# Kernel optimization log

Hardware: AMD Instinct MI355X
Metric: run time of the kernel (lower is better)

## Reference

```python
import jax, jax.numpy as jnp
import numpy as np

B, L, G, D = 32, 128, 64, 256
HD = 128; H = 2 * HD          # bidirectional LSTM hidden
N, K = 8, 4                   # nodes per graph, idx per node
NINP, NHID, NREL = 128, 32, 16
NTOK = 1000
E = B * N * N                 # all-pairs edges per graph, flattened
EPS = 1e-5


def setup_inputs() -> dict:
    key = jax.random.key(0)
    ks = jax.random.split(key, 40)
    rn = lambda i, shape, s: (s * jax.random.normal(ks[i], shape)).astype(jnp.float32)
    inp = {}
    inp["seq"] = jax.random.randint(ks[0], (B, L), 0, NTOK, dtype=jnp.int32)
    inp["pos2grp"] = jax.random.randint(ks[1], (B, L), 0, G, dtype=jnp.int32)
    inp["idx"] = jax.random.randint(ks[2], (B, N, K), 0, L, dtype=jnp.int32)
    ii = np.repeat(np.arange(N), N); jj = np.tile(np.arange(N), N)
    inp["u"] = jnp.asarray((np.arange(B)[:, None] * N + ii[None, :]).reshape(-1), dtype=jnp.int32)
    inp["v"] = jnp.asarray((np.arange(B)[:, None] * N + jj[None, :]).reshape(-1), dtype=jnp.int32)
    inp["mask"] = jax.random.uniform(ks[3], (E, NREL)) < 0.1
    inp["emb"] = rn(4, (NTOK, D), 1.0)
    # BiLSTM params (1 layer, 2 directions); gate order i,f,g,o
    inp["Wih_f"] = rn(5, (4 * HD, D), 0.05); inp["Whh_f"] = rn(6, (4 * HD, HD), 0.05)
    inp["bih_f"] = jnp.zeros((4 * HD,), jnp.float32); inp["bhh_f"] = jnp.zeros((4 * HD,), jnp.float32)
    inp["Wih_b"] = rn(7, (4 * HD, D), 0.05); inp["Whh_b"] = rn(8, (4 * HD, HD), 0.05)
    inp["bih_b"] = jnp.zeros((4 * HD,), jnp.float32); inp["bhh_b"] = jnp.zeros((4 * HD,), jnp.float32)
    inp["lin_src_w"] = rn(9, (NINP, H), 0.05); inp["lin_src_b"] = jnp.zeros((NINP,), jnp.float32)
    inp["lin_dst_w"] = rn(10, (NINP, H), 0.05); inp["lin_dst_b"] = jnp.zeros((NINP,), jnp.float32)
    inp["bn_src_g"] = jnp.ones((NINP,), jnp.float32); inp["bn_src_b"] = jnp.zeros((NINP,), jnp.float32)
    inp["bn_dst_g"] = jnp.ones((NINP,), jnp.float32); inp["bn_dst_b"] = jnp.zeros((NINP,), jnp.float32)
    inp["ntl_w"] = rn(11, (NREL, NHID, NINP, NINP), 0.001)
    inp["ntl_v"] = rn(12, (NREL, NHID, 2 * NINP), 0.001)
    inp["ntl_b"] = jnp.zeros((NREL, NHID, 1), jnp.float32)
    inp["ntl_u"] = rn(13, (NREL, 1, NHID), 0.001)
    inp["ntl_bn_g"] = jnp.ones((NREL * NHID,), jnp.float32)
    inp["ntl_bn_b"] = jnp.zeros((NREL * NHID,), jnp.float32)
    return inp


def _lstm(xs, Wih, Whh, bih, bhh):
    # xs: (T, B, D) -> (T, B, HD)
    nb = xs.shape[1]
    def step(carry, xt):
        h, c = carry
        g = xt @ Wih.T + h @ Whh.T + bih + bhh
        i, f, gg, o = jnp.split(g, 4, axis=-1)
        c = jax.nn.sigmoid(f) * c + jax.nn.sigmoid(i) * jnp.tanh(gg)
        h = jax.nn.sigmoid(o) * jnp.tanh(c)
        return (h, c), h
    init = (jnp.zeros((nb, HD), xs.dtype), jnp.zeros((nb, HD), xs.dtype))
    _, hs = jax.lax.scan(step, init, xs)
    return hs


def _bn(x, g, b):
    # training-mode BatchNorm1d over axis 0 (biased variance, as torch)
    m = x.mean(0)
    v = x.var(0)
    return (x - m) * jax.lax.rsqrt(v + EPS) * g + b


def _forward(emb, Wih_f, Whh_f, bih_f, bhh_f, Wih_b, Whh_b, bih_b, bhh_b,
             lin_src_w, lin_src_b, lin_dst_w, lin_dst_b,
             bn_src_g, bn_src_b, bn_dst_g, bn_dst_b,
             ntl_w, ntl_v, ntl_b, ntl_u, ntl_bn_g, ntl_bn_b,
             seq, pos2grp, idx, u, v):
    # 1) token embedding + scatter_sum into groups
    x_tok = emb[seq]                                         # (B,L,D)
    flat_ids = (pos2grp + jnp.arange(B, dtype=pos2grp.dtype)[:, None] * G).reshape(-1)
    x_grp = jax.ops.segment_sum(x_tok.reshape(B * L, D), flat_ids,
                                num_segments=B * G).reshape(B, G, D)
    # 2) BiLSTM over group sequence
    xs = x_grp.transpose(1, 0, 2)                            # (G,B,D)
    hf = _lstm(xs, Wih_f, Whh_f, bih_f, bhh_f)
    hb = _lstm(xs[::-1], Wih_b, Whh_b, bih_b, bhh_b)[::-1]
    h_grp = jnp.concatenate([hf, hb], -1).transpose(1, 0, 2) # (B,G,H)
    # 3) fancy-indexed gather h_grp[i, pos2grp[i, idx], :] + scatter_sum over K
    grp_of_idx = jnp.take_along_axis(pos2grp, idx.reshape(B, N * K), axis=1)
    h_sel = jnp.take_along_axis(h_grp, grp_of_idx[..., None], axis=1)  # (B,N*K,H)
    h = h_sel.reshape(B, N, K, H).sum(2).reshape(B * N, H)
    # 4) per-endpoint projection + batchnorm
    hd = _bn(h[u] @ lin_src_w.T + lin_src_b, bn_src_g, bn_src_b)  # (E,NINP)
    tl = _bn(h[v] @ lin_dst_w.T + lin_dst_b, bn_dst_g, bn_dst_b)
    # 5) neural tensor layer (bilinear=True)
    cat = jnp.concatenate([hd, tl], 1)                       # (E,2*NINP)
    linear = jnp.einsum('rhi,ei->rhe', ntl_v, cat)
    tmp = jnp.einsum('rhij,ei->rhej', ntl_w, hd)             # (NREL,NHID,E,NINP)
    bilinear = jnp.einsum('rhej,ej->rhe', tmp, tl)
    pre = bilinear + linear + ntl_b                          # (NREL,NHID,E)
    flat = pre.reshape(NREL * NHID, E).T                     # (E, NREL*NHID)
    act = jnp.tanh(_bn(flat, ntl_bn_g, ntl_bn_b).T.reshape(NREL, NHID, E))
    logit = jnp.einsum('rh,rhe->er', ntl_u[:, 0, :], act)    # (E,NREL)
    return logit


def reference(seq, pos2grp, idx, u, v, mask, emb,
              Wih_f, Whh_f, bih_f, bhh_f, Wih_b, Whh_b, bih_b, bhh_b,
              lin_src_w, lin_src_b, lin_dst_w, lin_dst_b,
              bn_src_g, bn_src_b, bn_dst_g, bn_dst_b,
              ntl_w, ntl_v, ntl_b, ntl_u, ntl_bn_g, ntl_bn_b):
    logit = _forward(emb, Wih_f, Whh_f, bih_f, bhh_f, Wih_b, Whh_b, bih_b, bhh_b,
                     lin_src_w, lin_src_b, lin_dst_w, lin_dst_b,
                     bn_src_g, bn_src_b, bn_dst_g, bn_dst_b,
                     ntl_w, ntl_v, ntl_b, ntl_u, ntl_bn_g, ntl_bn_b,
                     seq, pos2grp, idx, u, v)
    gt = logit > 0
    eq = gt == mask
    acc = eq.astype(jnp.float32).mean()
    gid = jnp.repeat(jnp.arange(B, dtype=jnp.int32), N * N)
    em = jax.ops.segment_min(jnp.all(eq, 1).astype(jnp.int32), gid, num_segments=B)
    emr = em.astype(jnp.float32).mean()
    nll_pos = -jnp.sum(jnp.where(mask, jax.nn.log_sigmoid(logit), 0.0)) / B
    nll_neg = -jnp.sum(jnp.where(mask, 0.0, jnp.log(1.0 + 1e-5 - jax.nn.sigmoid(logit)))) / B
    loss = nll_pos + nll_neg
    return logit, loss, acc, emr
```

## Files before the change

### kernel.cpp

```cpp
#include <hip/hip_runtime.h>
#include <math.h>

namespace {

constexpr int cB = 32, cL = 128, cG = 64, cD = 256;
constexpr int cHD = 128, cH = 256;
constexpr int cN = 8, cK = 4;
constexpr int cNI = 128, cRH = 512;
constexpr int cE = 2048;
constexpr float cEPS = 1e-5f;

typedef __bf16 bf16x8 __attribute__((ext_vector_type(8)));
typedef float f32x4 __attribute__((ext_vector_type(4)));

__device__ __forceinline__ f32x4 mfma16(bf16x8 a, bf16x8 b, f32x4 c) {
    return __builtin_amdgcn_mfma_f32_16x16x32_bf16(a, b, c, 0, 0, 0);
}

__device__ __forceinline__ float bf2f(unsigned short u) {
    unsigned int x = ((unsigned int)u) << 16;
    return __uint_as_float(x);
}
__device__ __forceinline__ unsigned short f2bf(float f) {
    unsigned int x = __float_as_uint(f);
    unsigned int r = (x + 0x7fffu + ((x >> 16) & 1u)) >> 16;
    return (unsigned short)r;
}
__device__ __forceinline__ float frcp(float x) { return __builtin_amdgcn_rcpf(x); }
__device__ __forceinline__ float fsig(float x) { return frcp(1.f + __expf(-x)); }
__device__ __forceinline__ float ftanh(float x) { return 1.f - 2.f * frcp(__expf(2.f * x) + 1.f); }
__device__ __forceinline__ float nls(float x) {
    return (x >= 0.f) ? log1pf(expf(-x)) : (log1pf(expf(x)) - x);
}

__device__ __forceinline__ void bar_lgkm() {
    asm volatile("s_waitcnt lgkmcnt(0)\n\ts_barrier" ::: "memory");
}

__global__ void k_embed(const int* __restrict__ seq, const int* __restrict__ p2g,
                        const float* __restrict__ emb, float* __restrict__ x_seq) {
    __shared__ float xl[cG * cD];
    int b = blockIdx.x, t = threadIdx.x;
    for (int g = 0; g < cG; ++g) xl[g * cD + t] = 0.f;
    for (int l = 0; l < cL; ++l) {
        int tok = seq[b * cL + l];
        int g = p2g[b * cL + l];
        xl[g * cD + t] += emb[tok * cD + t];
    }
    for (int g = 0; g < cG; ++g)
        x_seq[(g * cB + b) * cD + t] = xl[g * cD + t];
}

__global__ __launch_bounds__(256) void k_gemm_in(
    const float* __restrict__ x_seq,
    const float* __restrict__ wih_f, const float* __restrict__ wih_b,
    const float* __restrict__ bih_f, const float* __restrict__ bhh_f,
    const float* __restrict__ bih_b, const float* __restrict__ bhh_b,
    float* __restrict__ pre) {
    __shared__ float As[64][17];
    __shared__ float Bs[16][68];
    int t = threadIdx.x;
    int n0 = blockIdx.x * 64, m0 = blockIdx.y * 64;
    int tx = t & 15, ty = t >> 4;
    float acc[4][4] = {};
    for (int k0 = 0; k0 < cD; k0 += 16) {
        {
            int r = t >> 2, c = (t & 3) * 4;
            float4 a4 = *(const float4*)(x_seq + (size_t)(m0 + r) * cD + k0 + c);
            As[r][c + 0] = a4.x; As[r][c + 1] = a4.y; As[r][c + 2] = a4.z; As[r][c + 3] = a4.w;
        }
        {
            int n = t >> 2, c = (t & 3) * 4;
            int gn = n0 + n;
            const float* wrow = (gn < 512) ? (wih_f + (size_t)gn * cD)
                                           : (wih_b + (size_t)(gn - 512) * cD);
            float4 b4 = *(const float4*)(wrow + k0 + c);
            Bs[c + 0][n] = b4.x; Bs[c + 1][n] = b4.y; Bs[c + 2][n] = b4.z; Bs[c + 3][n] = b4.w;
        }
        __syncthreads();
#pragma unroll
        for (int k = 0; k < 16; ++k) {
            float a[4], bb[4];
#pragma unroll
            for (int i = 0; i < 4; ++i) a[i] = As[ty * 4 + i][k];
#pragma unroll
            for (int j = 0; j < 4; ++j) bb[j] = Bs[k][tx * 4 + j];
#pragma unroll
            for (int i = 0; i < 4; ++i)
#pragma unroll
                for (int j = 0; j < 4; ++j) acc[i][j] += a[i] * bb[j];
        }
        __syncthreads();
    }
#pragma unroll
    for (int i = 0; i < 4; ++i) {
        int m = m0 + ty * 4 + i;
        int g = m >> 5, b = m & 31;
        float4 v;
        float* vv = &v.x;
#pragma unroll
        for (int j = 0; j < 4; ++j) {
            int n = n0 + tx * 4 + j;
            float bias = (n < 512) ? (bih_f[n] + bhh_f[n]) : (bih_b[n - 512] + bhh_b[n - 512]);
            vv[j] = acc[i][j] + bias;
        }
        *(float4*)(pre + (((size_t)g * 256 + (n0 >> 2) + tx) * 32 + b) * 4) = v;
    }
}

__device__ __forceinline__ void lstm_step(
    f32x4 (&acc)[4], float (&cst)[4], const bf16x8 (&wf)[4][4],
    const unsigned short* __restrict__ hr, unsigned short* __restrict__ hw,
    const int (&rdo)[4], int wro,
    const float* __restrict__ preb, int gpre, bool dopre,
    unsigned short* __restrict__ hob, int g) {
    bf16x8 hf[4];
#pragma unroll
    for (int kf = 0; kf < 4; ++kf)
        hf[kf] = *(const bf16x8*)((const char*)hr + rdo[kf]);
#pragma unroll
    for (int kf = 0; kf < 4; ++kf)
#pragma unroll
        for (int q = 0; q < 4; ++q)
            acc[q] = mfma16(wf[q][kf], hf[kf], acc[q]);
    float hv[4];
#pragma unroll
    for (int r = 0; r < 4; ++r) {
        float ig = fsig(acc[0][r]);
        float fg = fsig(acc[1][r]);
        float gg = ftanh(acc[2][r]);
        float og = fsig(acc[3][r]);
        float cv = fg * cst[r] + ig * gg;
        cst[r] = cv;
        hv[r] = og * ftanh(cv);
    }
    if (dopre) {
#pragma unroll
        for (int q = 0; q < 4; ++q)
            acc[q] = *(const f32x4*)(preb + (size_t)gpre * 32768 + q * 4096);
    }
    unsigned int p0 = (unsigned int)f2bf(hv[0]) | ((unsigned int)f2bf(hv[1]) << 16);
    unsigned int p1 = (unsigned int)f2bf(hv[2]) | ((unsigned int)f2bf(hv[3]) << 16);
    *(uint2*)((char*)hw + wro) = make_uint2(p0, p1);
    *(uint2*)(hob + (size_t)g * 8192) = make_uint2(p0, p1);
    bar_lgkm();
}

__global__ __launch_bounds__(512, 2) void k_lstm_m(
    const float* __restrict__ pre,
    const float* __restrict__ whh_f, const float* __restrict__ whh_b,
    unsigned short* __restrict__ h_out) {
    __shared__ __align__(16) unsigned short hl[2][2048];
    int t = threadIdx.x;
    int w = t >> 6, l = t & 63, lc = l & 15, lk = l >> 4;
    int dir = blockIdx.x >> 1, bg = (blockIdx.x & 1) * 16;
    const float* whh = dir ? whh_b : whh_f;
    bf16x8 wf[4][4];
#pragma unroll
    for (int q = 0; q < 4; ++q) {
        int n = q * 128 + w * 16 + lc;
#pragma unroll
        for (int kf = 0; kf < 4; ++kf) {
            const float* src = whh + (size_t)n * 128 + kf * 32 + lk * 8;
            float4 s0 = *(const float4*)src, s1 = *(const float4*)(src + 4);
            bf16x8 v;
            v[0] = (__bf16)s0.x; v[1] = (__bf16)s0.y; v[2] = (__bf16)s0.z; v[3] = (__bf16)s0.w;
            v[4] = (__bf16)s1.x; v[5] = (__bf16)s1.y; v[6] = (__bf16)s1.z; v[7] = (__bf16)s1.w;
            wf[q][kf] = v;
        }
    }
    *(uint2*)&hl[1][t * 4] = make_uint2(0u, 0u);
    const float* preb = pre + ((size_t)(dir * 128 + w * 4 + lk) * 32 + (bg + lc)) * 4;
    unsigned short* hob = h_out + ((size_t)(dir * 32 + bg + lc) * 128 + w * 16 + lk * 4);
    int rdo[4];
#pragma unroll
    for (int kf = 0; kf < 4; ++kf)
        rdo[kf] = (lc * 256 + kf * 64 + lk * 16) ^ (lc << 4);
    int wro = (lc * 256 + w * 32 + lk * 8) ^ (lc << 4);
    f32x4 accA[4], accB[4];
    float cst[4] = {0.f, 0.f, 0.f, 0.f};
    int g0 = dir ? 63 : 0;
    int sgn = dir ? -1 : 1;
#pragma unroll
    for (int q = 0; q < 4; ++q) accA[q] = *(const f32x4*)(preb + (size_t)g0 * 32768 + q * 4096);
#pragma unroll
    for (int q = 0; q < 4; ++q) accB[q] = *(const f32x4*)(preb + (size_t)(g0 + sgn) * 32768 + q * 4096);
    bar_lgkm();
    for (int s = 0; s < 64; s += 2) {
        int ga = g0 + sgn * s;
        lstm_step(accA, cst, wf, hl[1], hl[0], rdo, wro, preb,
                  ga + 2 * sgn, s < 62, hob, ga);
        lstm_step(accB, cst, wf, hl[0], hl[1], rdo, wro, preb,
                  ga + 3 * sgn, s < 61, hob, ga + sgn);
    }
}

__global__ __launch_bounds__(256) void k_gather_proj(
    const int* __restrict__ idx, const int* __restrict__ p2g,
    const unsigned short* __restrict__ h_out,
    const float* __restrict__ w_src, const float* __restrict__ b_src,
    const float* __restrict__ w_dst, const float* __restrict__ b_dst,
    float* __restrict__ s_raw, float* __restrict__ d_raw) {
    int bn = blockIdx.x;
    int b = bn >> 3;
    int t = threadIdx.x;
    int dirq = t >> 7, hh = t & 127;
    __shared__ float xr[cH];
    float acc = 0.f;
#pragma unroll
    for (int k = 0; k < cK; ++k) {
        int l = idx[bn * cK + k];
        int g = p2g[b * cL + l];
        acc += bf2f(h_out[(size_t)g * 8192 + (size_t)(dirq * 32 + b) * 128 + hh]);
    }
    xr[t] = acc;
    __syncthreads();
    int which = t >> 7, c = t & 127;
    const float* w = which ? w_dst : w_src;
    const float* bb = which ? b_dst : b_src;
    const float* wr = w + (size_t)c * cH;
    float s = bb[c];
#pragma unroll 8
    for (int k = 0; k < cH; k += 4) {
        float4 w4 = *(const float4*)(wr + k);
        s += w4.x * xr[k] + w4.y * xr[k + 1] + w4.z * xr[k + 2] + w4.w * xr[k + 3];
    }
    (which ? d_raw : s_raw)[(size_t)bn * cNI + c] = s;
}

__global__ void k_bn_nodes(const float* __restrict__ s_raw, const float* __restrict__ d_raw,
                           const float* __restrict__ g_src, const float* __restrict__ b_src,
                           const float* __restrict__ g_dst, const float* __restrict__ b_dst,
                           float* __restrict__ hd_bn, float* __restrict__ tl_bn) {
    int ch = blockIdx.x, which = ch >> 7, cc = ch & 127;
    int t = threadIdx.x;
    const float* raw = which ? d_raw : s_raw;
    float v = raw[(size_t)t * cNI + cc];
    __shared__ float ssum[256], ssq[256];
    ssum[t] = v;
    ssq[t] = v * v;
    __syncthreads();
    for (int o = 128; o > 0; o >>= 1) {
        if (t < o) { ssum[t] += ssum[t + o]; ssq[t] += ssq[t + o]; }
        __syncthreads();
    }
    float mean = ssum[0] * (1.f / 256.f);
    float var = ssq[0] * (1.f / 256.f) - mean * mean;
    float gam = which ? g_dst[cc] : g_src[cc];
    float bet = which ? b_dst[cc] : b_src[cc];
    float scale = gam * rsqrtf(var + cEPS);
    (which ? tl_bn : hd_bn)[(size_t)t * cNI + cc] = (v - mean) * scale + bet;
}

__global__ __launch_bounds__(256, 2) void k_ntl_A(
    const float* __restrict__ hd_bn, const float* __restrict__ tl_bn,
    const float* __restrict__ ntl_w, const float* __restrict__ ntl_v,
    unsigned short* __restrict__ tmp,
    float* __restrict__ lsrc, float* __restrict__ ldst) {
    __shared__ __align__(16) unsigned short wl[128 * 128];
    __shared__ float vsh[256];
    int rh = blockIdx.x, t = threadIdx.x;
    int w = t >> 6, l = t & 63, lc = l & 15, lk = l >> 4;
    vsh[t] = ntl_v[(size_t)rh * 256 + t];
    {
        const float* wbase = ntl_w + (size_t)rh * 16384;
        int k = t >> 1, c0 = (t & 1) * 64;
        int sw = ((k >> 3) & 3) << 4;
#pragma unroll
        for (int u = 0; u < 8; ++u) {
            const float* src = wbase + k * 128 + c0 + u * 8;
            float4 f0 = *(const float4*)src, f1 = *(const float4*)(src + 4);
            bf16x8 v;
            v[0] = (__bf16)f0.x; v[1] = (__bf16)f0.y; v[2] = (__bf16)f0.z; v[3] = (__bf16)f0.w;
            v[4] = (__bf16)f1.x; v[5] = (__bf16)f1.y; v[6] = (__bf16)f1.z; v[7] = (__bf16)f1.w;
            *(bf16x8*)((char*)wl + ((k * 256 + (c0 + u * 8) * 2) ^ sw)) = v;
        }
    }
    __syncthreads();
    {
        const float* hr = hd_bn + (size_t)t * cNI;
        const float* tr = tl_bn + (size_t)t * cNI;
        float a1 = 0.f, a2 = 0.f;
#pragma unroll 8
        for (int i = 0; i < cNI; i += 4) {
            float4 h4 = *(const float4*)(hr + i);
            float4 t4 = *(const float4*)(tr + i);
            a1 += h4.x * vsh[i] + h4.y * vsh[i + 1] + h4.z * vsh[i + 2] + h4.w * vsh[i + 3];
            a2 += t4.x * vsh[128 + i] + t4.y * vsh[128 + i + 1] + t4.z * vsh[128 + i + 2] + t4.w * vsh[128 + i + 3];
        }
        lsrc[(size_t)rh * 256 + t] = a1;
        ldst[(size_t)rh * 256 + t] = a2;
    }
    f32x4 acc[4][8] = {};
#pragma unroll
    for (int kf = 0; kf < 4; ++kf) {
        bf16x8 af[4];
#pragma unroll
        for (int mt = 0; mt < 4; ++mt) {
            int m = w * 64 + mt * 16 + lc;
            const float* ap = hd_bn + (size_t)m * 128 + kf * 32 + lk * 8;
            float4 a0 = *(const float4*)ap, a1 = *(const float4*)(ap + 4);
            bf16x8 v;
            v[0] = (__bf16)a0.x; v[1] = (__bf16)a0.y; v[2] = (__bf16)a0.z; v[3] = (__bf16)a0.w;
            v[4] = (__bf16)a1.x; v[5] = (__bf16)a1.y; v[6] = (__bf16)a1.z; v[7] = (__bf16)a1.w;
            af[mt] = v;
        }
#pragma unroll
        for (int nt = 0; nt < 8; ++nt) {
            int kb = (kf * 32 + lk * 8) * 256;
            int jb = (nt * 16 + lc) * 2;
            bf16x8 bv = *(const bf16x8*)((char*)wl + ((kb + jb) ^ (lk << 4)));
#pragma unroll
            for (int mt = 0; mt < 4; ++mt) acc[mt][nt] = mfma16(af[mt], bv, acc[mt][nt]);
        }
    }
#pragma unroll
    for (int mt = 0; mt < 4; ++mt) {
#pragma unroll
        for (int nt = 0; nt < 8; ++nt) {
            unsigned int lo = (unsigned int)f2bf(acc[mt][nt][0]) | ((unsigned int)f2bf(acc[mt][nt][1]) << 16);
            unsigned int hi = (unsigned int)f2bf(acc[mt][nt][2]) | ((unsigned int)f2bf(acc[mt][nt][3]) << 16);
            size_t off = (size_t)rh * 32768 + (size_t)((((w * 4 + mt) * 8 + nt) * 64 + l) * 4);
            *(uint2*)(tmp + off) = make_uint2(lo, hi);
        }
    }
}

__global__ __launch_bounds__(256) void k_ntl_B(
    const unsigned short* __restrict__ tmp, const float* __restrict__ tl_bn,
    const float* __restrict__ lsrc, const float* __restrict__ ldst,
    const float* __restrict__ ntl_b, float* __restrict__ pre2) {
    int bgid = blockIdx.x;
    int rh = blockIdx.y;
    int t = threadIdx.x;
    int n0 = bgid * 32;
    __shared__ float tm[32][132];
    __shared__ float tl[32][132];
    {
        const uint4* src = (const uint4*)(tmp + (size_t)rh * 32768 +
                                          (size_t)(bgid >> 1) * 8192 + (size_t)(bgid & 1) * 4096);
#pragma unroll
        for (int rep = 0; rep < 2; ++rep) {
            int q = t + rep * 256;
            uint4 uv = src[q];
            unsigned int wds[4] = {uv.x, uv.y, uv.z, uv.w};
            int e0 = q * 8;
#pragma unroll
            for (int ui = 0; ui < 4; ++ui) {
                int e = e0 + ui * 2;
                int mt_l = e >> 11;
                int nt = (e >> 8) & 7;
                int ln = (e >> 2) & 63;
                int r = e & 3;
                int m = mt_l * 16 + (ln >> 4) * 4 + r;
                int j = nt * 16 + (ln & 15);
                tm[m][j] = bf2f((unsigned short)(wds[ui] & 0xffff));
                tm[m + 1][j] = bf2f((unsigned short)(wds[ui] >> 16));
            }
        }
        int r = t >> 3;
        int c0 = (t & 7) * 16;
        const float4* fsrc = (const float4*)(tl_bn + (size_t)(n0 + r) * cNI + c0);
        float4 f0 = fsrc[0], f1 = fsrc[1], f2v = fsrc[2], f3 = fsrc[3];
        float* frow = &tl[r][c0];
        frow[0] = f0.x; frow[1] = f0.y; frow[2] = f0.z; frow[3] = f0.w;
        frow[4] = f1.x; frow[5] = f1.y; frow[6] = f1.z; frow[7] = f1.w;
        frow[8] = f2v.x; frow[9] = f2v.y; frow[10] = f2v.z; frow[11] = f2v.w;
        frow[12] = f3.x; frow[13] = f3.y; frow[14] = f3.z; frow[15] = f3.w;
    }
    __syncthreads();
    int b_l = t >> 6, p = t & 63, i = p >> 3, j = p & 7;
    const float* ta = &tm[b_l * 8 + i][0];
    const float* tb = &tl[b_l * 8 + j][0];
    float s = 0.f;
#pragma unroll 8
    for (int k = 0; k < 128; ++k) s += ta[k] * tb[k];
    int e = bgid * 256 + t;
    int bglob = bgid * 4 + b_l;
    int un = bglob * 8 + i, vn = bglob * 8 + j;
    pre2[(size_t)rh * cE + e] = s + lsrc[(size_t)rh * 256 + un] + ldst[(size_t)rh * 256 + vn] + ntl_b[rh];
}

__global__ void k_bn2(const float* __restrict__ pre2,
                      const float* __restrict__ g, const float* __restrict__ bta,
                      float* __restrict__ scale, float* __restrict__ shift) {
    int rh = blockIdx.x, t = threadIdx.x;
    const float* row = pre2 + (size_t)rh * cE;
    float s = 0.f, q = 0.f;
#pragma unroll
    for (int ii = 0; ii < 8; ++ii) {
        float v = row[ii * 256 + t];
        s += v; q += v * v;
    }
    __shared__ float ssum[256], ssq[256];
    ssum[t] = s; ssq[t] = q;
    __syncthreads();
    for (int o = 128; o > 0; o >>= 1) {
        if (t < o) { ssum[t] += ssum[t + o]; ssq[t] += ssq[t + o]; }
        __syncthreads();
    }
    if (t == 0) {
        float mean = ssum[0] * (1.f / 2048.f);
        float var = ssq[0] * (1.f / 2048.f) - mean * mean;
        float sc = g[rh] * rsqrtf(var + cEPS);
        scale[rh] = sc;
        shift[rh] = bta[rh] - mean * sc;
    }
}

__global__ __launch_bounds__(256) void k_final(
    const float* __restrict__ pre2,
    const float* __restrict__ scale, const float* __restrict__ shift,
    const float* __restrict__ ntl_u, float* __restrict__ out) {
    int r = blockIdx.y;
    int e = blockIdx.x * 256 + threadIdx.x;
    float a = 0.f;
#pragma unroll
    for (int h = 0; h < 32; ++h) {
        int rh = r * 32 + h;
        float p = pre2[(size_t)rh * cE + e];
        a += ntl_u[rh] * ftanh(fmaf(p, scale[rh], shift[rh]));
    }
    out[(size_t)e * 16 + r] = a;
}

__global__ void k_loss(const float* __restrict__ out, const int* __restrict__ mask,
                       float* __restrict__ part) {
    int b = blockIdx.x, t = threadIdx.x;
    float nll = 0.f;
    int corr = 0, em = 1;
#pragma unroll
    for (int q = 0; q < 4; ++q) {
        int f = t * 4 + q;
        float x = out[(size_t)b * 1024 + f];
        int m = mask[(size_t)b * 1024 + f];
        bool gt = x > 0.f;
        bool mb = (m != 0);
        bool eq = (gt == mb);
        corr += eq ? 1 : 0;
        em &= eq ? 1 : 0;
        if (mb) nll += nls(x);
        else nll += -logf(1.f / (1.f + expf(x)) + 1e-5f);
    }
    __shared__ float rs[256];
    __shared__ int rc[256], re[256];
    rs[t] = nll; rc[t] = corr; re[t] = em;
    __syncthreads();
    for (int o = 128; o > 0; o >>= 1) {
        if (t < o) { rs[t] += rs[t + o]; rc[t] += rc[t + o]; re[t] &= re[t + o]; }
        __syncthreads();
    }
    if (t == 0) {
        part[b * 4 + 0] = rs[0];
        part[b * 4 + 1] = (float)rc[0];
        part[b * 4 + 2] = (float)re[0];
    }
}

__global__ void k_loss_fin(const float* __restrict__ part, float* __restrict__ out) {
    if (threadIdx.x == 0) {
        float nll = 0.f, corr = 0.f, em = 0.f;
        for (int b = 0; b < 32; ++b) {
            nll += part[b * 4 + 0];
            corr += part[b * 4 + 1];
            em += part[b * 4 + 2];
        }
        out[32768] = nll / 32.f;
        out[32769] = corr / 32768.f;
        out[32770] = em / 32.f;
    }
}

}

extern "C" void kernel_launch(void* const* d_in, const int* in_sizes, int n_in,
                              void* d_out, int out_size, void* d_ws, size_t ws_size,
                              hipStream_t stream) {
    (void)in_sizes; (void)n_in; (void)out_size; (void)ws_size;
    const int* seq = (const int*)d_in[0];
    const int* p2g = (const int*)d_in[1];
    const int* idx = (const int*)d_in[2];
    const int* mask = (const int*)d_in[5];
    const float* emb = (const float*)d_in[6];
    const float* wih_f = (const float*)d_in[7];
    const float* whh_f = (const float*)d_in[8];
    const float* bih_f = (const float*)d_in[9];
    const float* bhh_f = (const float*)d_in[10];
    const float* wih_b = (const float*)d_in[11];
    const float* whh_b = (const float*)d_in[12];
    const float* bih_b = (const float*)d_in[13];
    const float* bhh_b = (const float*)d_in[14];
    const float* lsw = (const float*)d_in[15];
    const float* lsb = (const float*)d_in[16];
    const float* ldw = (const float*)d_in[17];
    const float* ldb = (const float*)d_in[18];
    const float* bn_sg = (const float*)d_in[19];
    const float* bn_sb = (const float*)d_in[20];
    const float* bn_dg = (const float*)d_in[21];
    const float* bn_db = (const float*)d_in[22];
    const float* ntlw = (const float*)d_in[23];
    const float* ntlv = (const float*)d_in[24];
    const float* ntlb = (const float*)d_in[25];
    const float* ntlu = (const float*)d_in[26];
    const float* bn2g = (const float*)d_in[27];
    const float* bn2b = (const float*)d_in[28];
    float* out = (float*)d_out;
    char* ws = (char*)d_ws;

    float* x_seq = (float*)(ws + 0);
    float* pre = (float*)(ws + 2097152);
    unsigned short* tmp = (unsigned short*)(ws + 0);
    size_t off = 33554432;
    unsigned short* h_out = (unsigned short*)(ws + off); off += 1048576;
    float* s_raw = (float*)(ws + off); off += 131072;
    float* d_raw = (float*)(ws + off); off += 131072;
    float* hd_bn = (float*)(ws + off); off += 131072;
    float* tl_bn = (float*)(ws + off); off += 131072;
    float* lsrc = (float*)(ws + off); off += 524288;
    float* ldst = (float*)(ws + off); off += 524288;
    float* pre2 = (float*)(ws + off); off += 4194304;
    float* scale = (float*)(ws + off); off += 2048;
    float* shift = (float*)(ws + off); off += 2048;
    float* part = (float*)(ws + off); off += 512;

    k_embed<<<32, 256, 0, stream>>>(seq, p2g, emb, x_seq);
    k_gemm_in<<<dim3(16, 32), 256, 0, stream>>>(x_seq, wih_f, wih_b, bih_f, bhh_f, bih_b, bhh_b, pre);
    k_lstm_m<<<4, 512, 0, stream>>>(pre, whh_f, whh_b, h_out);
    k_gather_proj<<<256, 256, 0, stream>>>(idx, p2g, h_out, lsw, lsb, ldw, ldb, s_raw, d_raw);
    k_bn_nodes<<<256, 256, 0, stream>>>(s_raw, d_raw, bn_sg, bn_sb, bn_dg, bn_db, hd_bn, tl_bn);
    k_ntl_A<<<512, 256, 0, stream>>>(hd_bn, tl_bn, ntlw, ntlv, tmp, lsrc, ldst);
    k_ntl_B<<<dim3(8, 512), 256, 0, stream>>>(tmp, tl_bn, lsrc, ldst, ntlb, pre2);
    k_bn2<<<512, 256, 0, stream>>>(pre2, bn2g, bn2b, scale, shift);
    k_final<<<dim3(8, 16), 256, 0, stream>>>(pre2, scale, shift, ntlu, out);
    k_loss<<<32, 256, 0, stream>>>(out, mask, part);
    k_loss_fin<<<1, 32, 0, stream>>>(part, out);
}
```

Baseline: 183.2 us.

## Use MFMA for input GEMM, fuse projection with BN and loss into final kernel

The input-projection GEMM moves from a scalar FP32 LDS-tiled kernel to bf16 MFMA, with operands converted from global memory on the fly. The gather and projection are split into a transposed gather kernel and a per-channel projection kernel that also computes batch-norm statistics, which removes the separate BN kernel. The loss reduction is folded into k_final using wave ballots and shuffles, so the standalone loss kernel goes away. Together these cut kernel launches and scalar FP32 work, at the cost of bf16 rounding in the input GEMM and a gather stage that runs on only 8 blocks.

```diff
diff --git a/kernel.cpp b/kernel.cpp
--- a/kernel.cpp
+++ b/kernel.cpp
@@ -31,6 +31,13 @@
 __device__ __forceinline__ float ftanh(float x) { return 1.f - 2.f * frcp(__expf(2.f * x) + 1.f); }
 __device__ __forceinline__ float nls(float x) {
     return (x >= 0.f) ? log1pf(expf(-x)) : (log1pf(expf(x)) - x);
+}
+__device__ __forceinline__ bf16x8 cvt8(const float* __restrict__ p) {
+    float4 a = *(const float4*)p, b = *(const float4*)(p + 4);
+    bf16x8 v;
+    v[0] = (__bf16)a.x; v[1] = (__bf16)a.y; v[2] = (__bf16)a.z; v[3] = (__bf16)a.w;
+    v[4] = (__bf16)b.x; v[5] = (__bf16)b.y; v[6] = (__bf16)b.z; v[7] = (__bf16)b.w;
+    return v;
 }
 
 __device__ __forceinline__ void bar_lgkm() {
@@ -51,61 +58,46 @@
         x_seq[(g * cB + b) * cD + t] = xl[g * cD + t];
 }
 
-__global__ __launch_bounds__(256) void k_gemm_in(
+__global__ __launch_bounds__(512) void k_gemm_in(
     const float* __restrict__ x_seq,
     const float* __restrict__ wih_f, const float* __restrict__ wih_b,
     const float* __restrict__ bih_f, const float* __restrict__ bhh_f,
     const float* __restrict__ bih_b, const float* __restrict__ bhh_b,
     float* __restrict__ pre) {
-    __shared__ float As[64][17];
-    __shared__ float Bs[16][68];
+    int ns = blockIdx.x, g = blockIdx.y;
     int t = threadIdx.x;
-    int n0 = blockIdx.x * 64, m0 = blockIdx.y * 64;
-    int tx = t & 15, ty = t >> 4;
-    float acc[4][4] = {};
-    for (int k0 = 0; k0 < cD; k0 += 16) {
-        {
-            int r = t >> 2, c = (t & 3) * 4;
-            float4 a4 = *(const float4*)(x_seq + (size_t)(m0 + r) * cD + k0 + c);
-            As[r][c + 0] = a4.x; As[r][c + 1] = a4.y; As[r][c + 2] = a4.z; As[r][c + 3] = a4.w;
-        }
-        {
-            int n = t >> 2, c = (t & 3) * 4;
-            int gn = n0 + n;
-            const float* wrow = (gn < 512) ? (wih_f + (size_t)gn * cD)
-                                           : (wih_b + (size_t)(gn - 512) * cD);
-            float4 b4 = *(const float4*)(wrow + k0 + c);
-            Bs[c + 0][n] = b4.x; Bs[c + 1][n] = b4.y; Bs[c + 2][n] = b4.z; Bs[c + 3][n] = b4.w;
-        }
-        __syncthreads();
-#pragma unroll
-        for (int k = 0; k < 16; ++k) {
-            float a[4], bb[4];
-#pragma unroll
-            for (int i = 0; i < 4; ++i) a[i] = As[ty * 4 + i][k];
-#pragma unroll
-            for (int j = 0; j < 4; ++j) bb[j] = Bs[k][tx * 4 + j];
-#pragma unroll
-            for (int i = 0; i < 4; ++i)
-#pragma unroll
-                for (int j = 0; j < 4; ++j) acc[i][j] += a[i] * bb[j];
-        }
-        __syncthreads();
-    }
-#pragma unroll
-    for (int i = 0; i < 4; ++i) {
-        int m = m0 + ty * 4 + i;
-        int g = m >> 5, b = m & 31;
-        float4 v;
-        float* vv = &v.x;
-#pragma unroll
-        for (int j = 0; j < 4; ++j) {
-            int n = n0 + tx * 4 + j;
-            float bias = (n < 512) ? (bih_f[n] + bhh_f[n]) : (bih_b[n - 512] + bhh_b[n - 512]);
-            vv[j] = acc[i][j] + bias;
-        }
-        *(float4*)(pre + (((size_t)g * 256 + (n0 >> 2) + tx) * 32 + b) * 4) = v;
-    }
+    int w = t >> 6, l = t & 63, lc = l & 15, lk = l >> 4;
+    int gn = ns * 128 + w * 16 + lc;
+    const float* wrow = (gn < 512) ? (wih_f + (size_t)gn * cD)
+                                   : (wih_b + (size_t)(gn - 512) * cD);
+    const float* xb0 = x_seq + ((size_t)g * 32 + lc) * cD;
+    const float* xb1 = x_seq + ((size_t)g * 32 + 16 + lc) * cD;
+    f32x4 acc0 = {0.f, 0.f, 0.f, 0.f}, acc1 = {0.f, 0.f, 0.f, 0.f};
+#pragma unroll
+    for (int kf = 0; kf < 8; ++kf) {
+        int ko = kf * 32 + lk * 8;
+        bf16x8 a = cvt8(wrow + ko);
+        bf16x8 b0 = cvt8(xb0 + ko);
+        bf16x8 b1 = cvt8(xb1 + ko);
+        acc0 = mfma16(a, b0, acc0);
+        acc1 = mfma16(a, b1, acc1);
+    }
+    int nb = ns * 128 + w * 16 + lk * 4;
+    float4 bv;
+    if (nb < 512) {
+        float4 u = *(const float4*)(bih_f + nb);
+        float4 v = *(const float4*)(bhh_f + nb);
+        bv = make_float4(u.x + v.x, u.y + v.y, u.z + v.z, u.w + v.w);
+    } else {
+        float4 u = *(const float4*)(bih_b + nb - 512);
+        float4 v = *(const float4*)(bhh_b + nb - 512);
+        bv = make_float4(u.x + v.x, u.y + v.y, u.z + v.z, u.w + v.w);
+    }
+    size_t base = ((size_t)g * 256 + (nb >> 2)) * 32;
+    *(float4*)(pre + (base + lc) * 4) =
+        make_float4(acc0[0] + bv.x, acc0[1] + bv.y, acc0[2] + bv.z, acc0[3] + bv.w);
+    *(float4*)(pre + (base + 16 + lc) * 4) =
+        make_float4(acc1[0] + bv.x, acc1[1] + bv.y, acc1[2] + bv.z, acc1[3] + bv.w);
 }
 
 __device__ __forceinline__ void lstm_step(
@@ -160,14 +152,8 @@
     for (int q = 0; q < 4; ++q) {
         int n = q * 128 + w * 16 + lc;
 #pragma unroll
-        for (int kf = 0; kf < 4; ++kf) {
-            const float* src = whh + (size_t)n * 128 + kf * 32 + lk * 8;
-            float4 s0 = *(const float4*)src, s1 = *(const float4*)(src + 4);
-            bf16x8 v;
-            v[0] = (__bf16)s0.x; v[1] = (__bf16)s0.y; v[2] = (__bf16)s0.z; v[3] = (__bf16)s0.w;
-            v[4] = (__bf16)s1.x; v[5] = (__bf16)s1.y; v[6] = (__bf16)s1.z; v[7] = (__bf16)s1.w;
-            wf[q][kf] = v;
-        }
+        for (int kf = 0; kf < 4; ++kf)
+            wf[q][kf] = cvt8(whh + (size_t)n * 128 + kf * 32 + lk * 8);
     }
     *(uint2*)&hl[1][t * 4] = make_uint2(0u, 0u);
     const float* preb = pre + ((size_t)(dir * 128 + w * 4 + lk) * 32 + (bg + lc)) * 4;
@@ -188,57 +174,55 @@
     bar_lgkm();
     for (int s = 0; s < 64; s += 2) {
         int ga = g0 + sgn * s;
-        lstm_step(accA, cst, wf, hl[1], hl[0], rdo, wro, preb,
-                  ga + 2 * sgn, s < 62, hob, ga);
-        lstm_step(accB, cst, wf, hl[0], hl[1], rdo, wro, preb,
-                  ga + 3 * sgn, s < 61, hob, ga + sgn);
-    }
-}
-
-__global__ __launch_bounds__(256) void k_gather_proj(
+        lstm_step(accA, cst, wf, hl[1], hl[0], rdo, wro, preb, ga + 2 * sgn, s < 62, hob, ga);
+        lstm_step(accB, cst, wf, hl[0], hl[1], rdo, wro, preb, ga + 3 * sgn, s < 61, hob, ga + sgn);
+    }
+}
+
+__global__ __launch_bounds__(256) void k_gather(
     const int* __restrict__ idx, const int* __restrict__ p2g,
-    const unsigned short* __restrict__ h_out,
+    const unsigned short* __restrict__ h_out, float* __restrict__ hsumT) {
+    __shared__ float xr[32][257];
+    int n0 = blockIdx.x * 32, t = threadIdx.x;
+    int dirq = t >> 7, hh = t & 127;
+    for (int nl = 0; nl < 32; ++nl) {
+        int bn = n0 + nl;
+        int b = bn >> 3;
+        float acc = 0.f;
+#pragma unroll
+        for (int k = 0; k < cK; ++k) {
+            int l = idx[bn * cK + k];
+            int g = p2g[b * cL + l];
+            acc += bf2f(h_out[(size_t)g * 8192 + (size_t)(dirq * 32 + b) * 128 + hh]);
+        }
+        xr[nl][t] = acc;
+    }
+    __syncthreads();
+    int c_hi = t >> 5, nl = t & 31;
+    for (int rep = 0; rep < 32; ++rep) {
+        int c = rep * 8 + c_hi;
+        hsumT[(size_t)c * 256 + n0 + nl] = xr[nl][c];
+    }
+}
+
+__global__ __launch_bounds__(256) void k_proj_bn(
+    const float* __restrict__ hsumT,
     const float* __restrict__ w_src, const float* __restrict__ b_src,
     const float* __restrict__ w_dst, const float* __restrict__ b_dst,
-    float* __restrict__ s_raw, float* __restrict__ d_raw) {
-    int bn = blockIdx.x;
-    int b = bn >> 3;
-    int t = threadIdx.x;
-    int dirq = t >> 7, hh = t & 127;
-    __shared__ float xr[cH];
-    float acc = 0.f;
-#pragma unroll
-    for (int k = 0; k < cK; ++k) {
-        int l = idx[bn * cK + k];
-        int g = p2g[b * cL + l];
-        acc += bf2f(h_out[(size_t)g * 8192 + (size_t)(dirq * 32 + b) * 128 + hh]);
-    }
-    xr[t] = acc;
+    const float* __restrict__ g_src, const float* __restrict__ bb_src,
+    const float* __restrict__ g_dst, const float* __restrict__ bb_dst,
+    float* __restrict__ hd_bn, float* __restrict__ tl_bn) {
+    int which = blockIdx.x, c = blockIdx.y, t = threadIdx.x;
+    __shared__ float ws[256];
+    __shared__ float ssum[256], ssq[256];
+    ws[t] = (which ? w_dst : w_src)[(size_t)c * cH + t];
     __syncthreads();
-    int which = t >> 7, c = t & 127;
-    const float* w = which ? w_dst : w_src;
-    const float* bb = which ? b_dst : b_src;
-    const float* wr = w + (size_t)c * cH;
-    float s = bb[c];
+    float acc = (which ? b_dst : b_src)[c];
 #pragma unroll 8
-    for (int k = 0; k < cH; k += 4) {
-        float4 w4 = *(const float4*)(wr + k);
-        s += w4.x * xr[k] + w4.y * xr[k + 1] + w4.z * xr[k + 2] + w4.w * xr[k + 3];
-    }
-    (which ? d_raw : s_raw)[(size_t)bn * cNI + c] = s;
-}
-
-__global__ void k_bn_nodes(const float* __restrict__ s_raw, const float* __restrict__ d_raw,
-                           const float* __restrict__ g_src, const float* __restrict__ b_src,
-                           const float* __restrict__ g_dst, const float* __restrict__ b_dst,
-                           float* __restrict__ hd_bn, float* __restrict__ tl_bn) {
-    int ch = blockIdx.x, which = ch >> 7, cc = ch & 127;
-    int t = threadIdx.x;
-    const float* raw = which ? d_raw : s_raw;
-    float v = raw[(size_t)t * cNI + cc];
-    __shared__ float ssum[256], ssq[256];
-    ssum[t] = v;
-    ssq[t] = v * v;
+    for (int k = 0; k < cH; ++k)
+        acc += ws[k] * hsumT[(size_t)k * 256 + t];
+    ssum[t] = acc;
+    ssq[t] = acc * acc;
     __syncthreads();
     for (int o = 128; o > 0; o >>= 1) {
         if (t < o) { ssum[t] += ssum[t + o]; ssq[t] += ssq[t + o]; }
@@ -246,10 +230,10 @@
     }
     float mean = ssum[0] * (1.f / 256.f);
     float var = ssq[0] * (1.f / 256.f) - mean * mean;
-    float gam = which ? g_dst[cc] : g_src[cc];
-    float bet = which ? b_dst[cc] : b_src[cc];
+    float gam = which ? g_dst[c] : g_src[c];
+    float bet = which ? bb_dst[c] : bb_src[c];
     float scale = gam * rsqrtf(var + cEPS);
-    (which ? tl_bn : hd_bn)[(size_t)t * cNI + cc] = (v - mean) * scale + bet;
+    (which ? tl_bn : hd_bn)[(size_t)t * cNI + c] = (acc - mean) * scale + bet;
 }
 
 __global__ __launch_bounds__(256, 2) void k_ntl_A(
@@ -268,11 +252,7 @@
         int sw = ((k >> 3) & 3) << 4;
 #pragma unroll
         for (int u = 0; u < 8; ++u) {
-            const float* src = wbase + k * 128 + c0 + u * 8;
-            float4 f0 = *(const float4*)src, f1 = *(const float4*)(src + 4);
-            bf16x8 v;
-            v[0] = (__bf16)f0.x; v[1] = (__bf16)f0.y; v[2] = (__bf16)f0.z; v[3] = (__bf16)f0.w;
-            v[4] = (__bf16)f1.x; v[5] = (__bf16)f1.y; v[6] = (__bf16)f1.z; v[7] = (__bf16)f1.w;
+            bf16x8 v = cvt8(wbase + k * 128 + c0 + u * 8);
             *(bf16x8*)((char*)wl + ((k * 256 + (c0 + u * 8) * 2) ^ sw)) = v;
         }
     }
@@ -298,12 +278,7 @@
 #pragma unroll
         for (int mt = 0; mt < 4; ++mt) {
             int m = w * 64 + mt * 16 + lc;
-            const float* ap = hd_bn + (size_t)m * 128 + kf * 32 + lk * 8;
-            float4 a0 = *(const float4*)ap, a1 = *(const float4*)(ap + 4);
-            bf16x8 v;
-            v[0] = (__bf16)a0.x; v[1] = (__bf16)a0.y; v[2] = (__bf16)a0.z; v[3] = (__bf16)a0.w;
-            v[4] = (__bf16)a1.x; v[5] = (__bf16)a1.y; v[6] = (__bf16)a1.z; v[7] = (__bf16)a1.w;
-            af[mt] = v;
+            af[mt] = cvt8(hd_bn + (size_t)m * 128 + kf * 32 + lk * 8);
         }
 #pragma unroll
         for (int nt = 0; nt < 8; ++nt) {
@@ -411,9 +386,11 @@
 __global__ __launch_bounds__(256) void k_final(
     const float* __restrict__ pre2,
     const float* __restrict__ scale, const float* __restrict__ shift,
-    const float* __restrict__ ntl_u, float* __restrict__ out) {
-    int r = blockIdx.y;
-    int e = blockIdx.x * 256 + threadIdx.x;
+    const float* __restrict__ ntl_u, const int* __restrict__ mask,
+    float* __restrict__ out, float* __restrict__ part) {
+    int r = blockIdx.y, et = blockIdx.x;
+    int t = threadIdx.x;
+    int e = et * 256 + t;
     float a = 0.f;
 #pragma unroll
     for (int h = 0; h < 32; ++h) {
@@ -422,49 +399,42 @@
         a += ntl_u[rh] * ftanh(fmaf(p, scale[rh], shift[rh]));
     }
     out[(size_t)e * 16 + r] = a;
-}
-
-__global__ void k_loss(const float* __restrict__ out, const int* __restrict__ mask,
-                       float* __restrict__ part) {
-    int b = blockIdx.x, t = threadIdx.x;
-    float nll = 0.f;
-    int corr = 0, em = 1;
-#pragma unroll
-    for (int q = 0; q < 4; ++q) {
-        int f = t * 4 + q;
-        float x = out[(size_t)b * 1024 + f];
-        int m = mask[(size_t)b * 1024 + f];
-        bool gt = x > 0.f;
-        bool mb = (m != 0);
-        bool eq = (gt == mb);
-        corr += eq ? 1 : 0;
-        em &= eq ? 1 : 0;
-        if (mb) nll += nls(x);
-        else nll += -logf(1.f / (1.f + expf(x)) + 1e-5f);
-    }
-    __shared__ float rs[256];
-    __shared__ int rc[256], re[256];
-    rs[t] = nll; rc[t] = corr; re[t] = em;
-    __syncthreads();
-    for (int o = 128; o > 0; o >>= 1) {
-        if (t < o) { rs[t] += rs[t + o]; rc[t] += rc[t + o]; re[t] &= re[t + o]; }
-        __syncthreads();
+    int m = mask[(size_t)e * 16 + r];
+    bool mb = (m != 0);
+    bool eq = ((a > 0.f) == mb);
+    float nll = mb ? nls(a) : -logf(1.f / (1.f + expf(a)) + 1e-5f);
+    float corr = eq ? 1.f : 0.f;
+    unsigned long long bal = __ballot(eq);
+    float em = (bal == ~0ull) ? 1.f : 0.f;
+#pragma unroll
+    for (int o = 32; o > 0; o >>= 1) {
+        nll += __shfl_down(nll, o);
+        corr += __shfl_down(corr, o);
+    }
+    if ((t & 63) == 0) {
+        int bg = et * 4 + (t >> 6);
+        float* p = part + ((size_t)bg * 16 + r) * 4;
+        p[0] = nll; p[1] = corr; p[2] = em;
+    }
+}
+
+__global__ void k_loss_fin(const float* __restrict__ part, float* __restrict__ out) {
+    int t = threadIdx.x;
+    float nll = 0.f, corr = 0.f, em = 0.f;
+    if (t < 32) {
+        em = 1.f;
+        for (int r = 0; r < 16; ++r) {
+            const float* p = part + ((size_t)t * 16 + r) * 4;
+            nll += p[0]; corr += p[1]; em = fminf(em, p[2]);
+        }
+    }
+#pragma unroll
+    for (int o = 32; o > 0; o >>= 1) {
+        nll += __shfl_down(nll, o);
+        corr += __shfl_down(corr, o);
+        em += __shfl_down(em, o);
     }
     if (t == 0) {
-        part[b * 4 + 0] = rs[0];
-        part[b * 4 + 1] = (float)rc[0];
-        part[b * 4 + 2] = (float)re[0];
-    }
-}
-
-__global__ void k_loss_fin(const float* __restrict__ part, float* __restrict__ out) {
-    if (threadIdx.x == 0) {
-        float nll = 0.f, corr = 0.f, em = 0.f;
-        for (int b = 0; b < 32; ++b) {
-            nll += part[b * 4 + 0];
-            corr += part[b * 4 + 1];
-            em += part[b * 4 + 2];
-        }
         out[32768] = nll / 32.f;
         out[32769] = corr / 32768.f;
         out[32770] = em / 32.f;
@@ -512,8 +482,7 @@
     unsigned short* tmp = (unsigned short*)(ws + 0);
     size_t off = 33554432;
     unsigned short* h_out = (unsigned short*)(ws + off); off += 1048576;
-    float* s_raw = (float*)(ws + off); off += 131072;
-    float* d_raw = (float*)(ws + off); off += 131072;
+    float* hsumT = (float*)(ws + off); off += 262144;
     float* hd_bn = (float*)(ws + off); off += 131072;
     float* tl_bn = (float*)(ws + off); off += 131072;
     float* lsrc = (float*)(ws + off); off += 524288;
@@ -521,17 +490,17 @@
     float* pre2 = (float*)(ws + off); off += 4194304;
     float* scale = (float*)(ws + off); off += 2048;
     float* shift = (float*)(ws + off); off += 2048;
-    float* part = (float*)(ws + off); off += 512;
+    float* part = (float*)(ws + off); off += 8192;
 
     k_embed<<<32, 256, 0, stream>>>(seq, p2g, emb, x_seq);
-    k_gemm_in<<<dim3(16, 32), 256, 0, stream>>>(x_seq, wih_f, wih_b, bih_f, bhh_f, bih_b, bhh_b, pre);
+    k_gemm_in<<<dim3(8, 64), 512, 0, stream>>>(x_seq, wih_f, wih_b, bih_f, bhh_f, bih_b, bhh_b, pre);
     k_lstm_m<<<4, 512, 0, stream>>>(pre, whh_f, whh_b, h_out);
-    k_gather_proj<<<256, 256, 0, stream>>>(idx, p2g, h_out, lsw, lsb, ldw, ldb, s_raw, d_raw);
-    k_bn_nodes<<<256, 256, 0, stream>>>(s_raw, d_raw, bn_sg, bn_sb, bn_dg, bn_db, hd_bn, tl_bn);
+    k_gather<<<8, 256, 0, stream>>>(idx, p2g, h_out, hsumT);
+    k_proj_bn<<<dim3(2, 128), 256, 0, stream>>>(hsumT, lsw, lsb, ldw, ldb,
+                                                bn_sg, bn_sb, bn_dg, bn_db, hd_bn, tl_bn);
     k_ntl_A<<<512, 256, 0, stream>>>(hd_bn, tl_bn, ntlw, ntlv, tmp, lsrc, ldst);
     k_ntl_B<<<dim3(8, 512), 256, 0, stream>>>(tmp, tl_bn, lsrc, ldst, ntlb, pre2);
     k_bn2<<<512, 256, 0, stream>>>(pre2, bn2g, bn2b, scale, shift);
-    k_final<<<dim3(8, 16), 256, 0, stream>>>(pre2, scale, shift, ntlu, out);
-    k_loss<<<32, 256, 0, stream>>>(out, mask, part);
-    k_loss_fin<<<1, 32, 0, stream>>>(part, out);
-}
+    k_final<<<dim3(8, 16), 256, 0, stream>>>(pre2, scale, shift, ntlu, mask, out, part);
+    k_loss_fin<<<1, 64, 0, stream>>>(part, out);
+}
```

New measurement: 190.7 us. +4.1%, slower.
